# Kernel optimization log

Measured on AMD Instinct MI355X. Metric: run time of the kernel, lower is better.

## Reference

```python
import jax, jax.numpy as jnp
import numpy as np

B, T, H, K = 8192, 20, 128, 5


def setup_inputs() -> dict:
    key = jax.random.key(0)
    ks = jax.random.split(key, 20)
    n = jax.random.normal
    inp = {
        'cond_m': n(ks[0], (B, T, 2), jnp.float32),
        'cond_y': n(ks[1], (B, T, 1), jnp.float32),
        'cond_f': n(ks[2], (B, T, 1), jnp.float32),
        'cond_fadj': n(ks[3], (B, T, 1), jnp.float32),
        'state_h': n(ks[4], (B, H), jnp.float32) * 0.5,
        'state_c': n(ks[5], (B, H), jnp.float32) * 0.5,
        'W_my': n(ks[6], (H + 5, 4 * H), jnp.float32) * 0.05,
        'U_my': n(ks[7], (H, 4 * H), jnp.float32) * 0.05,
        'b_my': jnp.zeros((4 * H,), jnp.float32),
        'W_ff': n(ks[8], (H + 2, 4 * H), jnp.float32) * 0.05,
        'U_ff': n(ks[9], (H, 4 * H), jnp.float32) * 0.05,
        'b_ff': jnp.zeros((4 * H,), jnp.float32),
        'Wh_my': n(ks[10], (H, 9 * K), jnp.float32) * 0.1,
        'bh_my': jnp.zeros((9 * K,), jnp.float32),
        'Wh_ff': n(ks[11], (H, 6 * K), jnp.float32) * 0.1,
        'bh_ff': jnp.zeros((6 * K,), jnp.float32),
    }
    u = jax.random.uniform(ks[12], (T, 4, B, K), jnp.float32, 1e-6, 1.0 - 1e-6)
    inp['gumbel'] = -jnp.log(-jnp.log(u))
    inp['znorm'] = n(ks[13], (T, B, 5), jnp.float32)
    return inp


def reference(cond_m, cond_y, cond_f, cond_fadj, state_h, state_c,
              W_my, U_my, b_my, W_ff, U_ff, b_ff,
              Wh_my, bh_my, Wh_ff, bh_ff, gumbel, znorm):
    Kc = Wh_ff.shape[1] // 6
    allowed_m = jnp.asarray([0.3, 0.1], cond_m.dtype)  # merge vehicle allowed_error
    allowed_o = jnp.asarray(0.3, cond_m.dtype)         # other vehicles: allowed_error[0]
    enc_h = state_h  # constant encoder context fed every step

    def lstm_step(x, h, c, W, U, b):
        z = x @ W + h @ U + b
        i, f, g, o = jnp.split(z, 4, axis=-1)  # keras gate order i,f,c,o
        c2 = jax.nn.sigmoid(f) * c + jax.nn.sigmoid(i) * jnp.tanh(g)
        return jax.nn.sigmoid(o) * jnp.tanh(c2), c2

    def pick(p, idx):
        return jnp.take_along_axis(p, idx[:, None], axis=1)[:, 0]

    def step(carry, xs):
        h_my, c_my, h_ff, c_ff, cond5, cond2 = carry
        nm, ny, nf, nfa, g_t, z_t = xs
        h_my, c_my = lstm_step(jnp.concatenate([enc_h, cond5], -1), h_my, c_my, W_my, U_my, b_my)
        h_ff, c_ff = lstm_step(jnp.concatenate([enc_h, cond2], -1), h_ff, c_ff, W_ff, U_ff, b_ff)
        r_my = h_my @ Wh_my + bh_my  # fused 9 heads: [a_m,mu_l,s_l,mu_lat,s_lat,rho,a_y,mu_y,s_y]
        a_m = jax.nn.softmax(r_my[:, :Kc])
        mu_l = r_my[:, Kc:2 * Kc]
        s_l = jnp.exp(r_my[:, 2 * Kc:3 * Kc])
        mu_lat = r_my[:, 3 * Kc:4 * Kc]
        s_lat = jnp.exp(r_my[:, 4 * Kc:5 * Kc])
        rho = jnp.tanh(r_my[:, 5 * Kc:6 * Kc])
        a_y = jax.nn.softmax(r_my[:, 6 * Kc:7 * Kc])
        mu_y = r_my[:, 7 * Kc:8 * Kc]
        s_y = jnp.exp(r_my[:, 8 * Kc:9 * Kc])
        r_ff = h_ff @ Wh_ff + bh_ff  # fused 6 heads: [a_f,mu_f,s_f,a_fa,mu_fa,s_fa]
        a_f = jax.nn.softmax(r_ff[:, :Kc]); mu_f = r_ff[:, Kc:2 * Kc]; s_f = jnp.exp(r_ff[:, 2 * Kc:3 * Kc])
        a_fa = jax.nn.softmax(r_ff[:, 3 * Kc:4 * Kc]); mu_fa = r_ff[:, 4 * Kc:5 * Kc]; s_fa = jnp.exp(r_ff[:, 5 * Kc:6 * Kc])
        gp_m = jnp.concatenate([a_m, mu_l, s_l, mu_lat, s_lat, rho], -1)   # [B,30]
        gp_y = jnp.concatenate([a_y, mu_y, s_y], -1)                       # [B,15]
        gp_f = jnp.concatenate([a_f, mu_f, s_f], -1)
        gp_fa = jnp.concatenate([a_fa, mu_fa, s_fa], -1)
        # --- GMM sampling (gumbel-max component, reparameterized gaussian) ---
        idx_m = jnp.argmax(jnp.log(a_m) + g_t[0], -1)
        z1, z2 = z_t[:, 0], z_t[:, 1]
        r = pick(rho, idx_m)
        s_long = pick(mu_l, idx_m) + pick(s_l, idx_m) * z1
        s_lt = pick(mu_lat, idx_m) + pick(s_lat, idx_m) * (r * z1 + jnp.sqrt(1.0 - r * r) * z2)
        samp_m = jnp.stack([s_long, s_lt], -1)  # [B,2]
        def uni(a, mu, s, g, z):
            i = jnp.argmax(jnp.log(a) + g, -1)
            return pick(mu, i) + pick(s, i) * z
        samp_y = uni(a_y, mu_y, s_y, g_t[1], z_t[:, 2])
        samp_f = uni(a_f, mu_f, s_f, g_t[2], z_t[:, 3])
        samp_fa = uni(a_fa, mu_fa, s_fa, g_t[3], z_t[:, 4])
        # --- teacher forcing check: use sample when within allowed error ---
        cm = jnp.where(jnp.abs(samp_m - nm) < allowed_m, samp_m, nm)
        cy = jnp.where(jnp.abs(samp_y - ny) < allowed_o, samp_y, ny)
        cf = jnp.where(jnp.abs(samp_f - nf) < allowed_o, samp_f, nf)
        cfa = jnp.where(jnp.abs(samp_fa - nfa) < allowed_o, samp_fa, nfa)
        cond2_n = jnp.stack([cf, cfa], -1)
        cond5_n = jnp.concatenate([cm, cy[:, None], cond2_n], -1)
        return (h_my, c_my, h_ff, c_ff, cond5_n, cond2_n), (gp_m, gp_y, gp_f, gp_fa)

    cond5_0 = jnp.concatenate([cond_m[:, 0], cond_y[:, 0], cond_f[:, 0], cond_fadj[:, 0]], -1)
    cond2_0 = jnp.concatenate([cond_f[:, 0], cond_fadj[:, 0]], -1)
    shift = lambda c: jnp.concatenate([c[:, 1:], c[:, -1:]], 1)  # next-step targets; last pad unused
    xs = (jnp.transpose(shift(cond_m), (1, 0, 2)),
          shift(cond_y)[:, :, 0].T, shift(cond_f)[:, :, 0].T, shift(cond_fadj)[:, :, 0].T,
          gumbel, znorm)
    init = (state_h, state_c, state_h, state_c, cond5_0, cond2_0)
    _, (gm, gy, gf, gfa) = jax.lax.scan(step, init, xs)
    tr = lambda g: jnp.transpose(g, (1, 0, 2))  # [T,B,D] -> [B,T,D]
    return tr(gm), tr(gy), tr(gf), tr(gfa)
```

## Files before the change

### kernel.cpp

```cpp
#include <hip/hip_runtime.h>

#define BB 8192
#define TT 20
#define HH 128
#define H4 512
#define KC 5
#define R 32
#define NT 512
#define NBLK (BB/R)

typedef _Float16 f16;
typedef float v4f __attribute__((ext_vector_type(4)));
typedef _Float16 v8h __attribute__((ext_vector_type(8)));

#define GY_OFF (BB*TT*30)
#define GF_OFF (GY_OFF + BB*TT*15)
#define GFA_OFF (GF_OFF + BB*TT*15)

#define UMY_O   0
#define UFF_O   65536
#define WMYH_O  131072
#define WMYL_O  196608
#define WFFH_O  262144
#define WFFL_O  327680
#define WHMY_O  393216
#define WHFF_O  399360
#define PREP_N  272384

__device__ __forceinline__ float rcp_(float x){ return __builtin_amdgcn_rcpf(x); }
__device__ __forceinline__ float sigm(float x){ return rcp_(1.0f + __expf(-x)); }
__device__ __forceinline__ float tanh_(float x){
    x = __builtin_amdgcn_fmed3f(x, -10.0f, 10.0f);
    float e = __expf(2.0f * x);
    return (e - 1.0f) * rcp_(e + 1.0f);
}

#define AM0 0.3f
#define AM1 0.1f
#define AO  0.3f

__global__ void prep_kernel(const float* __restrict__ U_my, const float* __restrict__ U_ff,
                            const float* __restrict__ W_my, const float* __restrict__ W_ff,
                            const float* __restrict__ Wh_my, const float* __restrict__ Wh_ff,
                            f16* __restrict__ ws)
{
    int t = blockIdx.x * 256 + threadIdx.x;
    if (t >= PREP_N) return;
    if (t < 131072){
        int m = t >> 16, e = t & 65535;
        int jj = e & 7, L = (e >> 3) & 63, q = (e >> 9) & 3, c = e >> 11;
        int k   = q*32 + ((L >> 4) << 3) + jj;
        int col = (c & 3)*HH + ((c >> 2) << 4) + (L & 15);
        float v = (m ? U_ff : U_my)[k*H4 + col];
        ws[(m ? UFF_O : UMY_O) + e] = (f16)v;
    } else if (t < 262144){
        int m = (t - 131072) >> 16, e = t & 65535;
        int jj = e & 7, L = (e >> 3) & 63, q = (e >> 9) & 3, c = e >> 11;
        int k   = q*32 + ((L >> 4) << 3) + jj;
        int col = (c & 3)*HH + ((c >> 2) << 4) + (L & 15);
        float v = (m ? W_ff : W_my)[k*H4 + col];
        f16 hi = (f16)v;
        f16 lo = (f16)(v - (float)hi);
        ws[(m ? WFFH_O : WMYH_O) + e] = hi;
        ws[(m ? WFFL_O : WMYL_O) + e] = lo;
    } else if (t < 262144 + 6144){
        int e = t - 262144;
        int jj = e & 7, L = (e >> 3) & 63, q = (e >> 9) & 3, c = e >> 11;
        int k   = q*32 + ((L >> 4) << 3) + jj;
        int col = (c << 4) + (L & 15);
        float v = (col < 45) ? Wh_my[k*45 + col] : 0.0f;
        ws[WHMY_O + e] = (f16)v;
    } else {
        int e = t - 262144 - 6144;
        int jj = e & 7, L = (e >> 3) & 63, q = (e >> 9) & 3, c = e >> 11;
        int k   = q*32 + ((L >> 4) << 3) + jj;
        int col = (c << 4) + (L & 15);
        float v = (col < 30) ? Wh_ff[k*30 + col] : 0.0f;
        ws[WHFF_O + e] = (f16)v;
    }
}

__global__ __launch_bounds__(NT, 2) void decoder_kernel(
    const float* __restrict__ cond_m, const float* __restrict__ cond_y,
    const float* __restrict__ cond_f, const float* __restrict__ cond_fa,
    const float* __restrict__ state_h, const float* __restrict__ state_c,
    const float* __restrict__ W_my, const float* __restrict__ b_my,
    const float* __restrict__ W_ff, const float* __restrict__ b_ff,
    const float* __restrict__ bh_my, const float* __restrict__ bh_ff,
    const float* __restrict__ gum, const float* __restrict__ znorm,
    const f16* __restrict__ ws, float* __restrict__ out)
{
    __shared__ f16 s_hm_hi[2][R][136], s_hm_lo[2][R][136];
    __shared__ f16 s_hf_hi[2][R][136], s_hf_lo[2][R][136];
    __shared__ float s_wcm[5][H4], s_wcf[2][H4];
    __shared__ float s_r[R][76];
    __shared__ float s_red[R][8];
    __shared__ float s_c5[R][5], s_c2[R][2];
    __shared__ float s_gum[2][R][20], s_zn[2][R][5], s_nc[2][R][5];

    const int tid  = threadIdx.x;
    const int lane = tid & 63, w = tid >> 6;
    const int quad = lane >> 4, l15 = lane & 15;
    const int jcol = (w << 4) + l15;
    const int row0 = blockIdx.x * R;

    for (int p = tid; p < R*HH; p += NT){
        int r = p >> 7, k = p & 127;
        float v = state_h[(row0 + r)*HH + k];
        f16 hi = (f16)v, lo = (f16)(v - (float)hi);
        s_hm_hi[0][r][k] = hi; s_hm_lo[0][r][k] = lo;
        s_hf_hi[0][r][k] = hi; s_hf_lo[0][r][k] = lo;
    }
    for (int p = tid; p < 5*H4; p += NT) s_wcm[p >> 9][p & 511] = W_my[(HH + (p >> 9))*H4 + (p & 511)];
    for (int p = tid; p < 2*H4; p += NT) s_wcf[p >> 9][p & 511] = W_ff[(HH + (p >> 9))*H4 + (p & 511)];
    if (tid < R){
        int b = row0 + tid;
        float m0 = cond_m[(b*TT)*2 + 0], m1 = cond_m[(b*TT)*2 + 1];
        float y0 = cond_y[b*TT], f0 = cond_f[b*TT], fa0 = cond_fa[b*TT];
        s_c5[tid][0]=m0; s_c5[tid][1]=m1; s_c5[tid][2]=y0; s_c5[tid][3]=f0; s_c5[tid][4]=fa0;
        s_c2[tid][0]=f0; s_c2[tid][1]=fa0;
    }
    for (int i = tid; i < 960; i += NT){
        if (i < 640){
            int r = i/20, rem = i - r*20, j = rem/5, k = rem - j*5;
            s_gum[0][r][rem] = gum[(j*BB + row0 + r)*KC + k];
        } else if (i < 800){
            int e = i - 640, r = e/5, k = e - r*5;
            s_zn[0][r][k] = znorm[(row0 + r)*5 + k];
        } else {
            int e = i - 800, r = e/5, k = e - r*5;
            int b = row0 + r; int tn = 1;
            float v = (k==0) ? cond_m[(b*TT + tn)*2 + 0]
                    : (k==1) ? cond_m[(b*TT + tn)*2 + 1]
                    : (k==2) ? cond_y[b*TT + tn]
                    : (k==3) ? cond_f[b*TT + tn]
                    :          cond_fa[b*TT + tn];
            s_nc[0][r][k] = v;
        }
    }

    float c_my[8], c_ff[8];
    #pragma unroll
    for (int rt = 0; rt < 2; rt++)
        #pragma unroll
        for (int v = 0; v < 4; v++){
            int row = rt*16 + quad*4 + v;
            float cv = state_c[(row0 + row)*HH + jcol];
            c_my[rt*4+v] = cv; c_ff[rt*4+v] = cv;
        }
    __syncthreads();

    v4f pre_m[4][2], pre_f[4][2];
    #pragma unroll
    for (int ci = 0; ci < 4; ci++){
        #pragma unroll
        for (int rt = 0; rt < 2; rt++){ pre_m[ci][rt] = (v4f){0,0,0,0}; pre_f[ci][rt] = (v4f){0,0,0,0}; }
        #pragma unroll
        for (int q = 0; q < 4; q++){
            int off = (((w*4 + ci)*4 + q)*64 + lane)*8;
            v8h bmh = *(const v8h*)(ws + WMYH_O + off);
            v8h bml = *(const v8h*)(ws + WMYL_O + off);
            v8h bfh = *(const v8h*)(ws + WFFH_O + off);
            v8h bfl = *(const v8h*)(ws + WFFL_O + off);
            #pragma unroll
            for (int rt = 0; rt < 2; rt++){
                v8h ahi = *(const v8h*)&s_hm_hi[0][rt*16 + l15][q*32 + quad*8];
                v8h alo = *(const v8h*)&s_hm_lo[0][rt*16 + l15][q*32 + quad*8];
                pre_m[ci][rt] = __builtin_amdgcn_mfma_f32_16x16x32_f16(ahi, bmh, pre_m[ci][rt],0,0,0);
                pre_m[ci][rt] = __builtin_amdgcn_mfma_f32_16x16x32_f16(ahi, bml, pre_m[ci][rt],0,0,0);
                pre_m[ci][rt] = __builtin_amdgcn_mfma_f32_16x16x32_f16(alo, bmh, pre_m[ci][rt],0,0,0);
                pre_f[ci][rt] = __builtin_amdgcn_mfma_f32_16x16x32_f16(ahi, bfh, pre_f[ci][rt],0,0,0);
                pre_f[ci][rt] = __builtin_amdgcn_mfma_f32_16x16x32_f16(ahi, bfl, pre_f[ci][rt],0,0,0);
                pre_f[ci][rt] = __builtin_amdgcn_mfma_f32_16x16x32_f16(alo, bfh, pre_f[ci][rt],0,0,0);
            }
        }
        float bmv = b_my[ci*HH + jcol], bfv = b_ff[ci*HH + jcol];
        #pragma unroll
        for (int rt = 0; rt < 2; rt++)
            #pragma unroll
            for (int v = 0; v < 4; v++){ pre_m[ci][rt][v] += bmv; pre_f[ci][rt][v] += bfv; }
    }

    v8h BUm[4][4], BUf[4][4];
    #pragma unroll
    for (int ci = 0; ci < 4; ci++)
        #pragma unroll
        for (int q = 0; q < 4; q++){
            int off = (((w*4 + ci)*4 + q)*64 + lane)*8;
            BUm[ci][q] = *(const v8h*)(ws + UMY_O + off);
            BUf[ci][q] = *(const v8h*)(ws + UFF_O + off);
        }

    int cur = 0;
    for (int t = 0; t < TT; t++){
        const int pb = t & 1;
        const f16 (*hmh)[136] = s_hm_hi[cur], (*hml)[136] = s_hm_lo[cur];
        const f16 (*hfh)[136] = s_hf_hi[cur], (*hfl)[136] = s_hf_lo[cur];
        f16 (*hmh_n)[136] = s_hm_hi[cur^1];  f16 (*hml_n)[136] = s_hm_lo[cur^1];
        f16 (*hfh_n)[136] = s_hf_hi[cur^1];  f16 (*hfl_n)[136] = s_hf_lo[cur^1];
        v4f am[2][4];

        #pragma unroll
        for (int rt = 0; rt < 2; rt++){
            #pragma unroll
            for (int ci = 0; ci < 4; ci++) am[rt][ci] = pre_m[ci][rt];
            #pragma unroll
            for (int q = 0; q < 4; q++){
                v8h ahi = *(const v8h*)&hmh[rt*16 + l15][q*32 + quad*8];
                v8h alo = *(const v8h*)&hml[rt*16 + l15][q*32 + quad*8];
                #pragma unroll
                for (int ci = 0; ci < 4; ci++){
                    am[rt][ci] = __builtin_amdgcn_mfma_f32_16x16x32_f16(ahi, BUm[ci][q], am[rt][ci],0,0,0);
                    am[rt][ci] = __builtin_amdgcn_mfma_f32_16x16x32_f16(alo, BUm[ci][q], am[rt][ci],0,0,0);
                }
            }
        }

        #pragma unroll
        for (int rt = 0; rt < 2; rt++)
            #pragma unroll
            for (int v = 0; v < 4; v++){
                int row = rt*16 + quad*4 + v;
                float z0 = am[rt][0][v], z1 = am[rt][1][v], z2 = am[rt][2][v], z3 = am[rt][3][v];
                #pragma unroll
                for (int k = 0; k < 5; k++){
                    float cv = s_c5[row][k];
                    z0 = fmaf(cv, s_wcm[k][0*HH + jcol], z0);
                    z1 = fmaf(cv, s_wcm[k][1*HH + jcol], z1);
                    z2 = fmaf(cv, s_wcm[k][2*HH + jcol], z2);
                    z3 = fmaf(cv, s_wcm[k][3*HH + jcol], z3);
                }
                float c2 = sigm(z1)*c_my[rt*4+v] + sigm(z0)*tanh_(z2);
                c_my[rt*4+v] = c2;
                float h = sigm(z3)*tanh_(c2);
                f16 hi = (f16)h;
                hmh_n[row][jcol] = hi;
                hml_n[row][jcol] = (f16)(h - (float)hi);
            }

        #pragma unroll
        for (int rt = 0; rt < 2; rt++){
            #pragma unroll
            for (int ci = 0; ci < 4; ci++) am[rt][ci] = pre_f[ci][rt];
            #pragma unroll
            for (int q = 0; q < 4; q++){
                v8h ahi = *(const v8h*)&hfh[rt*16 + l15][q*32 + quad*8];
                v8h alo = *(const v8h*)&hfl[rt*16 + l15][q*32 + quad*8];
                #pragma unroll
                for (int ci = 0; ci < 4; ci++){
                    am[rt][ci] = __builtin_amdgcn_mfma_f32_16x16x32_f16(ahi, BUf[ci][q], am[rt][ci],0,0,0);
                    am[rt][ci] = __builtin_amdgcn_mfma_f32_16x16x32_f16(alo, BUf[ci][q], am[rt][ci],0,0,0);
                }
            }
        }

        #pragma unroll
        for (int rt = 0; rt < 2; rt++)
            #pragma unroll
            for (int v = 0; v < 4; v++){
                int row = rt*16 + quad*4 + v;
                float z0 = am[rt][0][v], z1 = am[rt][1][v], z2 = am[rt][2][v], z3 = am[rt][3][v];
                #pragma unroll
                for (int k = 0; k < 2; k++){
                    float cv = s_c2[row][k];
                    z0 = fmaf(cv, s_wcf[k][0*HH + jcol], z0);
                    z1 = fmaf(cv, s_wcf[k][1*HH + jcol], z1);
                    z2 = fmaf(cv, s_wcf[k][2*HH + jcol], z2);
                    z3 = fmaf(cv, s_wcf[k][3*HH + jcol], z3);
                }
                float c2 = sigm(z1)*c_ff[rt*4+v] + sigm(z0)*tanh_(z2);
                c_ff[rt*4+v] = c2;
                float h = sigm(z3)*tanh_(c2);
                f16 hi = (f16)h;
                hfh_n[row][jcol] = hi;
                hfl_n[row][jcol] = (f16)(h - (float)hi);
            }
        __syncthreads();

        if (w < 5){
            const f16 (*Hhi)[136] = (w < 3) ? hmh_n : hfh_n;
            const f16 (*Hlo)[136] = (w < 3) ? hml_n : hfl_n;
            int base  = (w < 3) ? WHMY_O : WHFF_O;
            int ch    = (w < 3) ? w : w - 3;
            int ncol  = (w < 3) ? 45 : 30;
            int rbase = (w < 3) ? 0 : 45;
            const float* bh = (w < 3) ? bh_my : bh_ff;
            v8h BH[4];
            #pragma unroll
            for (int q = 0; q < 4; q++)
                BH[q] = *(const v8h*)(ws + base + ((ch*4 + q)*64 + lane)*8);
            int gc = ch*16 + l15;
            #pragma unroll
            for (int rt = 0; rt < 2; rt++){
                v4f a = (v4f){0,0,0,0};
                #pragma unroll
                for (int q = 0; q < 4; q++){
                    v8h ahi = *(const v8h*)&Hhi[rt*16 + l15][q*32 + quad*8];
                    v8h alo = *(const v8h*)&Hlo[rt*16 + l15][q*32 + quad*8];
                    a = __builtin_amdgcn_mfma_f32_16x16x32_f16(ahi, BH[q], a,0,0,0);
                    a = __builtin_amdgcn_mfma_f32_16x16x32_f16(alo, BH[q], a,0,0,0);
                }
                if (gc < ncol){
                    float bias = bh[gc];
                    #pragma unroll
                    for (int v = 0; v < 4; v++)
                        s_r[rt*16 + quad*4 + v][rbase + gc] = a[v] + bias;
                }
            }
        } else {
            int tp = t + 1;
            if (tp < TT){
                int pb2 = tp & 1;
                int tn2 = (tp + 1 < TT) ? tp + 1 : TT - 1;
                for (int i = tid - 320; i < 960; i += 192){
                    if (i < 640){
                        int r = i/20, rem = i - r*20, j = rem/5, k = rem - j*5;
                        s_gum[pb2][r][rem] = gum[((tp*4 + j)*BB + row0 + r)*KC + k];
                    } else if (i < 800){
                        int e = i - 640, r = e/5, k = e - r*5;
                        s_zn[pb2][r][k] = znorm[(tp*BB + row0 + r)*5 + k];
                    } else {
                        int e = i - 800, r = e/5, k = e - r*5;
                        int b = row0 + r;
                        float v = (k==0) ? cond_m[(b*TT + tn2)*2 + 0]
                                : (k==1) ? cond_m[(b*TT + tn2)*2 + 1]
                                : (k==2) ? cond_y[b*TT + tn2]
                                : (k==3) ? cond_f[b*TT + tn2]
                                :          cond_fa[b*TT + tn2];
                        s_nc[pb2][r][k] = v;
                    }
                }
            }
        }
        __syncthreads();

        if (tid < R*4){
            int r = tid >> 2, g = tid & 3;
            int base = (g==0) ? 0 : (g==1) ? 30 : (g==2) ? 45 : 60;
            float m = s_r[r][base];
            #pragma unroll
            for (int k = 1; k < KC; k++) m = fmaxf(m, s_r[r][base+k]);
            float s = 0.f;
            #pragma unroll
            for (int k = 0; k < KC; k++) s += __expf(s_r[r][base+k] - m);
            s_red[r][2*g] = m; s_red[r][2*g+1] = rcp_(s);
        } else if (tid < 2*R*4){
            int qq = tid - R*4;
            int r = qq >> 2, g = qq & 3;
            const float* Rr = s_r[r];
            int base = (g==0) ? 0 : (g==1) ? 30 : (g==2) ? 45 : 60;
            const float* gg = &s_gum[pb][r][g*5];
            int im = 0; float bv = Rr[base] + gg[0];
            #pragma unroll
            for (int k = 1; k < KC; k++){
                float v = Rr[base+k] + gg[k];
                if (v > bv){ bv = v; im = k; }
            }
            if (g == 0){
                float z1 = s_zn[pb][r][0], z2 = s_zn[pb][r][1];
                float rv   = tanh_(Rr[25 + im]);
                float slon = Rr[5 + im]  + __expf(Rr[10 + im]) * z1;
                float slat = Rr[15 + im] + __expf(Rr[20 + im]) *
                             (rv*z1 + sqrtf(fmaxf(0.f, 1.f - rv*rv))*z2);
                float nm0 = s_nc[pb][r][0], nm1 = s_nc[pb][r][1];
                s_c5[r][0] = (fabsf(slon - nm0) < AM0) ? slon : nm0;
                s_c5[r][1] = (fabsf(slat - nm1) < AM1) ? slat : nm1;
            } else if (g == 1){
                float sy = Rr[35 + im] + __expf(Rr[40 + im]) * s_zn[pb][r][2];
                float ny = s_nc[pb][r][2];
                s_c5[r][2] = (fabsf(sy - ny) < AO) ? sy : ny;
            } else if (g == 2){
                float sf = Rr[50 + im] + __expf(Rr[55 + im]) * s_zn[pb][r][3];
                float nf = s_nc[pb][r][3];
                float cf = (fabsf(sf - nf) < AO) ? sf : nf;
                s_c5[r][3] = cf; s_c2[r][0] = cf;
            } else {
                float sfa = Rr[65 + im] + __expf(Rr[70 + im]) * s_zn[pb][r][4];
                float nfa = s_nc[pb][r][4];
                float cfa = (fabsf(sfa - nfa) < AO) ? sfa : nfa;
                s_c5[r][4] = cfa; s_c2[r][1] = cfa;
            }
        }
        __syncthreads();

        {
            int r  = tid >> 4;
            int q0 = tid & 15;
            const float* Rr = s_r[r];
            int b = row0 + r;
            for (int q = q0; q < 75; q += 16){
                float v; int dst;
                if (q < 30){
                    float x = Rr[q];
                    if (q < 5)       v = __expf(x - s_red[r][0]) * s_red[r][1];
                    else if (q < 10) v = x;
                    else if (q < 15) v = __expf(x);
                    else if (q < 20) v = x;
                    else if (q < 25) v = __expf(x);
                    else             v = tanh_(x);
                    dst = (b*TT + t)*30 + q;
                } else if (q < 45){
                    int q2 = q - 30; float x = Rr[30 + q2];
                    v = (q2 < 5) ? __expf(x - s_red[r][2]) * s_red[r][3]
                                 : (q2 < 10) ? x : __expf(x);
                    dst = GY_OFF + (b*TT + t)*15 + q2;
                } else if (q < 60){
                    int q2 = q - 45; float x = Rr[45 + q2];
                    v = (q2 < 5) ? __expf(x - s_red[r][4]) * s_red[r][5]
                                 : (q2 < 10) ? x : __expf(x);
                    dst = GF_OFF + (b*TT + t)*15 + q2;
                } else {
                    int q2 = q - 60; float x = Rr[60 + q2];
                    v = (q2 < 5) ? __expf(x - s_red[r][6]) * s_red[r][7]
                                 : (q2 < 10) ? x : __expf(x);
                    dst = GFA_OFF + (b*TT + t)*15 + q2;
                }
                out[dst] = v;
            }
        }
        cur ^= 1;
    }
}

extern "C" void kernel_launch(void* const* d_in, const int* in_sizes, int n_in,
                              void* d_out, int out_size, void* d_ws, size_t ws_size,
                              hipStream_t stream)
{
    (void)in_sizes; (void)n_in; (void)ws_size; (void)out_size;
    const float* cond_m  = (const float*)d_in[0];
    const float* cond_y  = (const float*)d_in[1];
    const float* cond_f  = (const float*)d_in[2];
    const float* cond_fa = (const float*)d_in[3];
    const float* state_h = (const float*)d_in[4];
    const float* state_c = (const float*)d_in[5];
    const float* W_my    = (const float*)d_in[6];
    const float* U_my    = (const float*)d_in[7];
    const float* b_my    = (const float*)d_in[8];
    const float* W_ff    = (const float*)d_in[9];
    const float* U_ff    = (const float*)d_in[10];
    const float* b_ff    = (const float*)d_in[11];
    const float* Wh_my   = (const float*)d_in[12];
    const float* bh_my   = (const float*)d_in[13];
    const float* Wh_ff   = (const float*)d_in[14];
    const float* bh_ff   = (const float*)d_in[15];
    const float* gum     = (const float*)d_in[16];
    const float* znorm   = (const float*)d_in[17];
    f16* ws = (f16*)d_ws;
    float* out = (float*)d_out;

    prep_kernel<<<(PREP_N + 255)/256, 256, 0, stream>>>(U_my, U_ff, W_my, W_ff, Wh_my, Wh_ff, ws);
    decoder_kernel<<<NBLK, NT, 0, stream>>>(
        cond_m, cond_y, cond_f, cond_fa, state_h, state_c,
        W_my, b_my, W_ff, b_ff, bh_my, bh_ff, gum, znorm, ws, out);
}
```

Baseline: 422.1 us.

## Split my and ff LSTM cells across separate wave groups with 1024 threads

Doubles the block to 1024 threads so waves 0-7 compute the merge-vehicle LSTM and waves 8-15 the follower LSTM concurrently, instead of each wave doing both serially. The cell state moves from registers to shared memory, the head projection is spread over 10 waves, one per row-tile, and the output loop is widened to 32 threads per row. It also switches gumbel/znorm loads and output stores to nontemporal hints. The aim is to halve per-wave serial MFMA and gate work per step and free registers. The cost is extra shared-memory traffic for the cell state and more LDS per block, which may limit how many blocks fit per CU.

New measurement: 446.3 us. 5.7% more time.

```diff
diff --git a/kernel.cpp b/kernel.cpp
--- a/kernel.cpp
+++ b/kernel.cpp
@@ -6,7 +6,7 @@
 #define H4 512
 #define KC 5
 #define R 32
-#define NT 512
+#define NT 1024
 #define NBLK (BB/R)
 
 typedef _Float16 f16;
@@ -80,7 +80,35 @@
     }
 }
 
-__global__ __launch_bounds__(NT, 2) void decoder_kernel(
+template<int NC>
+__device__ __forceinline__ void gates_body(
+    const v4f am[4], const float* __restrict__ cndp, const float* __restrict__ wcp,
+    float* __restrict__ cst, f16 (* __restrict__ wr_hi)[136], f16 (* __restrict__ wr_lo)[136],
+    int rt, int quad, int jcol)
+{
+    #pragma unroll
+    for (int v = 0; v < 4; v++){
+        int row = rt*16 + quad*4 + v;
+        float z0 = am[0][v], z1 = am[1][v], z2 = am[2][v], z3 = am[3][v];
+        #pragma unroll
+        for (int k = 0; k < NC; k++){
+            float cv = cndp[row*NC + k];
+            z0 = fmaf(cv, wcp[k*H4 + 0*HH + jcol], z0);
+            z1 = fmaf(cv, wcp[k*H4 + 1*HH + jcol], z1);
+            z2 = fmaf(cv, wcp[k*H4 + 2*HH + jcol], z2);
+            z3 = fmaf(cv, wcp[k*H4 + 3*HH + jcol], z3);
+        }
+        float co = cst[row*132 + jcol];
+        float c2 = sigm(z1)*co + sigm(z0)*tanh_(z2);
+        cst[row*132 + jcol] = c2;
+        float h = sigm(z3)*tanh_(c2);
+        f16 hi = (f16)h;
+        wr_hi[row][jcol] = hi;
+        wr_lo[row][jcol] = (f16)(h - (float)hi);
+    }
+}
+
+__global__ __launch_bounds__(NT, 4) void decoder_kernel(
     const float* __restrict__ cond_m, const float* __restrict__ cond_y,
     const float* __restrict__ cond_f, const float* __restrict__ cond_fa,
     const float* __restrict__ state_h, const float* __restrict__ state_c,
@@ -93,6 +121,7 @@
     __shared__ f16 s_hm_hi[2][R][136], s_hm_lo[2][R][136];
     __shared__ f16 s_hf_hi[2][R][136], s_hf_lo[2][R][136];
     __shared__ float s_wcm[5][H4], s_wcf[2][H4];
+    __shared__ float s_cm[R][132], s_cf[R][132];
     __shared__ float s_r[R][76];
     __shared__ float s_red[R][8];
     __shared__ float s_c5[R][5], s_c2[R][2];
@@ -101,7 +130,9 @@
     const int tid  = threadIdx.x;
     const int lane = tid & 63, w = tid >> 6;
     const int quad = lane >> 4, l15 = lane & 15;
-    const int jcol = (w << 4) + l15;
+    const int stripe = w & 7;
+    const int isMy = (w < 8);
+    const int jcol = (stripe << 4) + l15;
     const int row0 = blockIdx.x * R;
 
     for (int p = tid; p < R*HH; p += NT){
@@ -110,6 +141,11 @@
         f16 hi = (f16)v, lo = (f16)(v - (float)hi);
         s_hm_hi[0][r][k] = hi; s_hm_lo[0][r][k] = lo;
         s_hf_hi[0][r][k] = hi; s_hf_lo[0][r][k] = lo;
+    }
+    for (int p = tid; p < R*HH; p += NT){
+        int r = p >> 7, k = p & 127;
+        float cv = state_c[(row0 + r)*HH + k];
+        s_cm[r][k] = cv; s_cf[r][k] = cv;
     }
     for (int p = tid; p < 5*H4; p += NT) s_wcm[p >> 9][p & 511] = W_my[(HH + (p >> 9))*H4 + (p & 511)];
     for (int p = tid; p < 2*H4; p += NT) s_wcf[p >> 9][p & 511] = W_ff[(HH + (p >> 9))*H4 + (p & 511)];
@@ -123,10 +159,10 @@
     for (int i = tid; i < 960; i += NT){
         if (i < 640){
             int r = i/20, rem = i - r*20, j = rem/5, k = rem - j*5;
-            s_gum[0][r][rem] = gum[(j*BB + row0 + r)*KC + k];
+            s_gum[0][r][rem] = __builtin_nontemporal_load(&gum[(j*BB + row0 + r)*KC + k]);
         } else if (i < 800){
             int e = i - 640, r = e/5, k = e - r*5;
-            s_zn[0][r][k] = znorm[(row0 + r)*5 + k];
+            s_zn[0][r][k] = __builtin_nontemporal_load(&znorm[(row0 + r)*5 + k]);
         } else {
             int e = i - 800, r = e/5, k = e - r*5;
             int b = row0 + r; int tn = 1;
@@ -138,187 +174,118 @@
             s_nc[0][r][k] = v;
         }
     }
-
-    float c_my[8], c_ff[8];
-    #pragma unroll
-    for (int rt = 0; rt < 2; rt++)
+    __syncthreads();
+
+    v4f pre[4][2];
+    {
+        const int baseH = isMy ? WMYH_O : WFFH_O;
+        const int baseL = isMy ? WMYL_O : WFFL_O;
+        const float* bias = isMy ? b_my : b_ff;
         #pragma unroll
-        for (int v = 0; v < 4; v++){
-            int row = rt*16 + quad*4 + v;
-            float cv = state_c[(row0 + row)*HH + jcol];
-            c_my[rt*4+v] = cv; c_ff[rt*4+v] = cv;
-        }
-    __syncthreads();
-
-    v4f pre_m[4][2], pre_f[4][2];
-    #pragma unroll
-    for (int ci = 0; ci < 4; ci++){
+        for (int ci = 0; ci < 4; ci++){
+            pre[ci][0] = (v4f){0,0,0,0}; pre[ci][1] = (v4f){0,0,0,0};
+            #pragma unroll
+            for (int q = 0; q < 4; q++){
+                int off = (((stripe*4 + ci)*4 + q)*64 + lane)*8;
+                v8h bh_ = *(const v8h*)(ws + baseH + off);
+                v8h bl_ = *(const v8h*)(ws + baseL + off);
+                #pragma unroll
+                for (int rt = 0; rt < 2; rt++){
+                    v8h ahi = *(const v8h*)&s_hm_hi[0][rt*16 + l15][q*32 + quad*8];
+                    v8h alo = *(const v8h*)&s_hm_lo[0][rt*16 + l15][q*32 + quad*8];
+                    pre[ci][rt] = __builtin_amdgcn_mfma_f32_16x16x32_f16(ahi, bh_, pre[ci][rt],0,0,0);
+                    pre[ci][rt] = __builtin_amdgcn_mfma_f32_16x16x32_f16(ahi, bl_, pre[ci][rt],0,0,0);
+                    pre[ci][rt] = __builtin_amdgcn_mfma_f32_16x16x32_f16(alo, bh_, pre[ci][rt],0,0,0);
+                }
+            }
+            float bv = bias[ci*HH + jcol];
+            #pragma unroll
+            for (int rt = 0; rt < 2; rt++)
+                #pragma unroll
+                for (int v = 0; v < 4; v++) pre[ci][rt][v] += bv;
+        }
+    }
+
+    v8h BU[4][4];
+    {
+        const int ubase = isMy ? UMY_O : UFF_O;
         #pragma unroll
-        for (int rt = 0; rt < 2; rt++){ pre_m[ci][rt] = (v4f){0,0,0,0}; pre_f[ci][rt] = (v4f){0,0,0,0}; }
-        #pragma unroll
-        for (int q = 0; q < 4; q++){
-            int off = (((w*4 + ci)*4 + q)*64 + lane)*8;
-            v8h bmh = *(const v8h*)(ws + WMYH_O + off);
-            v8h bml = *(const v8h*)(ws + WMYL_O + off);
-            v8h bfh = *(const v8h*)(ws + WFFH_O + off);
-            v8h bfl = *(const v8h*)(ws + WFFL_O + off);
-            #pragma unroll
-            for (int rt = 0; rt < 2; rt++){
-                v8h ahi = *(const v8h*)&s_hm_hi[0][rt*16 + l15][q*32 + quad*8];
-                v8h alo = *(const v8h*)&s_hm_lo[0][rt*16 + l15][q*32 + quad*8];
-                pre_m[ci][rt] = __builtin_amdgcn_mfma_f32_16x16x32_f16(ahi, bmh, pre_m[ci][rt],0,0,0);
-                pre_m[ci][rt] = __builtin_amdgcn_mfma_f32_16x16x32_f16(ahi, bml, pre_m[ci][rt],0,0,0);
-                pre_m[ci][rt] = __builtin_amdgcn_mfma_f32_16x16x32_f16(alo, bmh, pre_m[ci][rt],0,0,0);
-                pre_f[ci][rt] = __builtin_amdgcn_mfma_f32_16x16x32_f16(ahi, bfh, pre_f[ci][rt],0,0,0);
-                pre_f[ci][rt] = __builtin_amdgcn_mfma_f32_16x16x32_f16(ahi, bfl, pre_f[ci][rt],0,0,0);
-                pre_f[ci][rt] = __builtin_amdgcn_mfma_f32_16x16x32_f16(alo, bfh, pre_f[ci][rt],0,0,0);
-            }
-        }
-        float bmv = b_my[ci*HH + jcol], bfv = b_ff[ci*HH + jcol];
-        #pragma unroll
-        for (int rt = 0; rt < 2; rt++)
-            #pragma unroll
-            for (int v = 0; v < 4; v++){ pre_m[ci][rt][v] += bmv; pre_f[ci][rt][v] += bfv; }
-    }
-
-    v8h BUm[4][4], BUf[4][4];
-    #pragma unroll
-    for (int ci = 0; ci < 4; ci++)
-        #pragma unroll
-        for (int q = 0; q < 4; q++){
-            int off = (((w*4 + ci)*4 + q)*64 + lane)*8;
-            BUm[ci][q] = *(const v8h*)(ws + UMY_O + off);
-            BUf[ci][q] = *(const v8h*)(ws + UFF_O + off);
-        }
+        for (int ci = 0; ci < 4; ci++)
+            #pragma unroll
+            for (int q = 0; q < 4; q++)
+                BU[ci][q] = *(const v8h*)(ws + ubase + (((stripe*4 + ci)*4 + q)*64 + lane)*8);
+    }
+
+    const float* wcp  = isMy ? &s_wcm[0][0] : &s_wcf[0][0];
+    const float* cndp = isMy ? &s_c5[0][0]  : &s_c2[0][0];
+    float*       cst  = isMy ? &s_cm[0][0]  : &s_cf[0][0];
 
     int cur = 0;
     for (int t = 0; t < TT; t++){
         const int pb = t & 1;
-        const f16 (*hmh)[136] = s_hm_hi[cur], (*hml)[136] = s_hm_lo[cur];
-        const f16 (*hfh)[136] = s_hf_hi[cur], (*hfl)[136] = s_hf_lo[cur];
-        f16 (*hmh_n)[136] = s_hm_hi[cur^1];  f16 (*hml_n)[136] = s_hm_lo[cur^1];
-        f16 (*hfh_n)[136] = s_hf_hi[cur^1];  f16 (*hfl_n)[136] = s_hf_lo[cur^1];
-        v4f am[2][4];
+        const f16 (*rd_hi)[136] = isMy ? s_hm_hi[cur]   : s_hf_hi[cur];
+        const f16 (*rd_lo)[136] = isMy ? s_hm_lo[cur]   : s_hf_lo[cur];
+        f16 (*wr_hi)[136]       = isMy ? s_hm_hi[cur^1] : s_hf_hi[cur^1];
+        f16 (*wr_lo)[136]       = isMy ? s_hm_lo[cur^1] : s_hf_lo[cur^1];
 
         #pragma unroll
         for (int rt = 0; rt < 2; rt++){
-            #pragma unroll
-            for (int ci = 0; ci < 4; ci++) am[rt][ci] = pre_m[ci][rt];
+            v4f am[4];
+            #pragma unroll
+            for (int ci = 0; ci < 4; ci++) am[ci] = pre[ci][rt];
             #pragma unroll
             for (int q = 0; q < 4; q++){
-                v8h ahi = *(const v8h*)&hmh[rt*16 + l15][q*32 + quad*8];
-                v8h alo = *(const v8h*)&hml[rt*16 + l15][q*32 + quad*8];
+                v8h ahi = *(const v8h*)&rd_hi[rt*16 + l15][q*32 + quad*8];
+                v8h alo = *(const v8h*)&rd_lo[rt*16 + l15][q*32 + quad*8];
                 #pragma unroll
                 for (int ci = 0; ci < 4; ci++){
-                    am[rt][ci] = __builtin_amdgcn_mfma_f32_16x16x32_f16(ahi, BUm[ci][q], am[rt][ci],0,0,0);
-                    am[rt][ci] = __builtin_amdgcn_mfma_f32_16x16x32_f16(alo, BUm[ci][q], am[rt][ci],0,0,0);
+                    am[ci] = __builtin_amdgcn_mfma_f32_16x16x32_f16(ahi, BU[ci][q], am[ci],0,0,0);
+                    am[ci] = __builtin_amdgcn_mfma_f32_16x16x32_f16(alo, BU[ci][q], am[ci],0,0,0);
                 }
             }
-        }
-
-        #pragma unroll
-        for (int rt = 0; rt < 2; rt++)
-            #pragma unroll
-            for (int v = 0; v < 4; v++){
-                int row = rt*16 + quad*4 + v;
-                float z0 = am[rt][0][v], z1 = am[rt][1][v], z2 = am[rt][2][v], z3 = am[rt][3][v];
+            if (isMy) gates_body<5>(am, cndp, wcp, cst, wr_hi, wr_lo, rt, quad, jcol);
+            else      gates_body<2>(am, cndp, wcp, cst, wr_hi, wr_lo, rt, quad, jcol);
+        }
+        __syncthreads();
+
+        if (w < 10){
+            int w5 = w >> 1, rth = w & 1;
+            int hm = (w5 < 3);
+            const f16 (*Hhi)[136] = hm ? s_hm_hi[cur^1] : s_hf_hi[cur^1];
+            const f16 (*Hlo)[136] = hm ? s_hm_lo[cur^1] : s_hf_lo[cur^1];
+            int base  = hm ? WHMY_O : WHFF_O;
+            int ch    = hm ? w5 : w5 - 3;
+            int ncol  = hm ? 45 : 30;
+            int rbase = hm ? 0 : 45;
+            const float* bh = hm ? bh_my : bh_ff;
+            v4f a = (v4f){0,0,0,0};
+            #pragma unroll
+            for (int q = 0; q < 4; q++){
+                v8h BHq = *(const v8h*)(ws + base + ((ch*4 + q)*64 + lane)*8);
+                v8h ahi = *(const v8h*)&Hhi[rth*16 + l15][q*32 + quad*8];
+                v8h alo = *(const v8h*)&Hlo[rth*16 + l15][q*32 + quad*8];
+                a = __builtin_amdgcn_mfma_f32_16x16x32_f16(ahi, BHq, a,0,0,0);
+                a = __builtin_amdgcn_mfma_f32_16x16x32_f16(alo, BHq, a,0,0,0);
+            }
+            int gc = ch*16 + l15;
+            if (gc < ncol){
+                float bias = bh[gc];
                 #pragma unroll
-                for (int k = 0; k < 5; k++){
-                    float cv = s_c5[row][k];
-                    z0 = fmaf(cv, s_wcm[k][0*HH + jcol], z0);
-                    z1 = fmaf(cv, s_wcm[k][1*HH + jcol], z1);
-                    z2 = fmaf(cv, s_wcm[k][2*HH + jcol], z2);
-                    z3 = fmaf(cv, s_wcm[k][3*HH + jcol], z3);
-                }
-                float c2 = sigm(z1)*c_my[rt*4+v] + sigm(z0)*tanh_(z2);
-                c_my[rt*4+v] = c2;
-                float h = sigm(z3)*tanh_(c2);
-                f16 hi = (f16)h;
-                hmh_n[row][jcol] = hi;
-                hml_n[row][jcol] = (f16)(h - (float)hi);
-            }
-
-        #pragma unroll
-        for (int rt = 0; rt < 2; rt++){
-            #pragma unroll
-            for (int ci = 0; ci < 4; ci++) am[rt][ci] = pre_f[ci][rt];
-            #pragma unroll
-            for (int q = 0; q < 4; q++){
-                v8h ahi = *(const v8h*)&hfh[rt*16 + l15][q*32 + quad*8];
-                v8h alo = *(const v8h*)&hfl[rt*16 + l15][q*32 + quad*8];
-                #pragma unroll
-                for (int ci = 0; ci < 4; ci++){
-                    am[rt][ci] = __builtin_amdgcn_mfma_f32_16x16x32_f16(ahi, BUf[ci][q], am[rt][ci],0,0,0);
-                    am[rt][ci] = __builtin_amdgcn_mfma_f32_16x16x32_f16(alo, BUf[ci][q], am[rt][ci],0,0,0);
-                }
-            }
-        }
-
-        #pragma unroll
-        for (int rt = 0; rt < 2; rt++)
-            #pragma unroll
-            for (int v = 0; v < 4; v++){
-                int row = rt*16 + quad*4 + v;
-                float z0 = am[rt][0][v], z1 = am[rt][1][v], z2 = am[rt][2][v], z3 = am[rt][3][v];
-                #pragma unroll
-                for (int k = 0; k < 2; k++){
-                    float cv = s_c2[row][k];
-                    z0 = fmaf(cv, s_wcf[k][0*HH + jcol], z0);
-                    z1 = fmaf(cv, s_wcf[k][1*HH + jcol], z1);
-                    z2 = fmaf(cv, s_wcf[k][2*HH + jcol], z2);
-                    z3 = fmaf(cv, s_wcf[k][3*HH + jcol], z3);
-                }
-                float c2 = sigm(z1)*c_ff[rt*4+v] + sigm(z0)*tanh_(z2);
-                c_ff[rt*4+v] = c2;
-                float h = sigm(z3)*tanh_(c2);
-                f16 hi = (f16)h;
-                hfh_n[row][jcol] = hi;
-                hfl_n[row][jcol] = (f16)(h - (float)hi);
-            }
-        __syncthreads();
-
-        if (w < 5){
-            const f16 (*Hhi)[136] = (w < 3) ? hmh_n : hfh_n;
-            const f16 (*Hlo)[136] = (w < 3) ? hml_n : hfl_n;
-            int base  = (w < 3) ? WHMY_O : WHFF_O;
-            int ch    = (w < 3) ? w : w - 3;
-            int ncol  = (w < 3) ? 45 : 30;
-            int rbase = (w < 3) ? 0 : 45;
-            const float* bh = (w < 3) ? bh_my : bh_ff;
-            v8h BH[4];
-            #pragma unroll
-            for (int q = 0; q < 4; q++)
-                BH[q] = *(const v8h*)(ws + base + ((ch*4 + q)*64 + lane)*8);
-            int gc = ch*16 + l15;
-            #pragma unroll
-            for (int rt = 0; rt < 2; rt++){
-                v4f a = (v4f){0,0,0,0};
-                #pragma unroll
-                for (int q = 0; q < 4; q++){
-                    v8h ahi = *(const v8h*)&Hhi[rt*16 + l15][q*32 + quad*8];
-                    v8h alo = *(const v8h*)&Hlo[rt*16 + l15][q*32 + quad*8];
-                    a = __builtin_amdgcn_mfma_f32_16x16x32_f16(ahi, BH[q], a,0,0,0);
-                    a = __builtin_amdgcn_mfma_f32_16x16x32_f16(alo, BH[q], a,0,0,0);
-                }
-                if (gc < ncol){
-                    float bias = bh[gc];
-                    #pragma unroll
-                    for (int v = 0; v < 4; v++)
-                        s_r[rt*16 + quad*4 + v][rbase + gc] = a[v] + bias;
-                }
+                for (int v = 0; v < 4; v++)
+                    s_r[rth*16 + quad*4 + v][rbase + gc] = a[v] + bias;
             }
         } else {
             int tp = t + 1;
             if (tp < TT){
                 int pb2 = tp & 1;
                 int tn2 = (tp + 1 < TT) ? tp + 1 : TT - 1;
-                for (int i = tid - 320; i < 960; i += 192){
+                for (int i = tid - 640; i < 960; i += 384){
                     if (i < 640){
                         int r = i/20, rem = i - r*20, j = rem/5, k = rem - j*5;
-                        s_gum[pb2][r][rem] = gum[((tp*4 + j)*BB + row0 + r)*KC + k];
+                        s_gum[pb2][r][rem] = __builtin_nontemporal_load(&gum[((tp*4 + j)*BB + row0 + r)*KC + k]);
                     } else if (i < 800){
                         int e = i - 640, r = e/5, k = e - r*5;
-                        s_zn[pb2][r][k] = znorm[(tp*BB + row0 + r)*5 + k];
+                        s_zn[pb2][r][k] = __builtin_nontemporal_load(&znorm[(tp*BB + row0 + r)*5 + k]);
                     } else {
                         int e = i - 800, r = e/5, k = e - r*5;
                         int b = row0 + r;
@@ -384,11 +351,11 @@
         __syncthreads();
 
         {
-            int r  = tid >> 4;
-            int q0 = tid & 15;
+            int r  = tid >> 5;
+            int q0 = tid & 31;
             const float* Rr = s_r[r];
             int b = row0 + r;
-            for (int q = q0; q < 75; q += 16){
+            for (int q = q0; q < 75; q += 32){
                 float v; int dst;
                 if (q < 30){
                     float x = Rr[q];
@@ -415,7 +382,7 @@
                                  : (q2 < 10) ? x : __expf(x);
                     dst = GFA_OFF + (b*TT + t)*15 + q2;
                 }
-                out[dst] = v;
+                __builtin_nontemporal_store(v, &out[dst]);
             }
         }
         cur ^= 1;
```
